# Performance work log

Measured on AMD Instinct MI355X. Metric: run time of the kernel, lower is better.

The kernel has to match this reference:

```python
import jax, jax.numpy as jnp
import numpy as np
from jax import lax

DN = ('NCHW', 'OIHW', 'NCHW')


def conv_s2(x, w, b):
    # Conv2d(kernel=4, stride=2, padding=1): halves H,W
    y = lax.conv_general_dilated(x, w, (2, 2), ((1, 1), (1, 1)), dimension_numbers=DN)
    return y + b[None, :, None, None]


def conv_1x1(x, w, b):
    y = lax.conv_general_dilated(x, w, (1, 1), ((0, 0), (0, 0)), dimension_numbers=DN)
    return y + b[None, :, None, None]


def convT_s2(x, w, b):
    # torch ConvTranspose2d(kernel=4, stride=2, padding=1); torch weight layout [I,O,kh,kw]
    wt = jnp.flip(w, (2, 3)).transpose(1, 0, 2, 3)  # -> [O,I,kh,kw], spatially flipped
    y = lax.conv_general_dilated(x, wt, (1, 1), ((2, 2), (2, 2)),
                                 lhs_dilation=(2, 2), dimension_numbers=DN)
    return y + b[None, :, None, None]


def setup_inputs() -> dict:
    key = jax.random.key(0)
    ks = jax.random.split(key, 20)
    f32 = jnp.float32
    s = 0.05  # small init scale to keep activations sane
    inp = {
        'x': jax.random.uniform(ks[0], (32, 3, 256, 256), dtype=f32),
        # encoder
        'ew1': jax.random.normal(ks[1], (128, 3, 4, 4), f32) * s,
        'eb1': jnp.zeros((128,), f32),
        'ew2': jax.random.normal(ks[2], (256, 128, 4, 4), f32) * s,
        'eb2': jnp.zeros((256,), f32),
        'ew3': jax.random.normal(ks[3], (512, 256, 4, 4), f32) * s,
        'eb3': jnp.zeros((512,), f32),
        # pre-VQ 1x1 conv
        'pw': jax.random.normal(ks[4], (64, 512, 1, 1), f32) * s,
        'pb': jnp.zeros((64,), f32),
        # codebook (torch.randn in module)
        'emb': jax.random.normal(ks[5], (512, 64), f32),
        # decoder (ConvTranspose2d weights: [in, out, kh, kw])
        'dw1': jax.random.normal(ks[6], (64, 256, 4, 4), f32) * s,
        'db1': jnp.zeros((256,), f32),
        'dw2': jax.random.normal(ks[7], (256, 128, 4, 4), f32) * s,
        'db2': jnp.zeros((128,), f32),
        'dw3': jax.random.normal(ks[8], (128, 3, 4, 4), f32) * s,
        'db3': jnp.zeros((3,), f32),
    }
    return inp


def reference(x, ew1, eb1, ew2, eb2, ew3, eb3, pw, pb, emb,
              dw1, db1, dw2, db2, dw3, db3):
    # encoder
    h = jax.nn.relu(conv_s2(x, ew1, eb1))
    h = jax.nn.relu(conv_s2(h, ew2, eb2))
    h = jax.nn.relu(conv_s2(h, ew3, eb3))
    z_e = conv_1x1(h, pw, pb)  # [B, D, H, W]

    b, d, hh, ww = z_e.shape
    x_flat = z_e.reshape(b, d, hh * ww).transpose(0, 2, 1)  # [B, HW, D]
    # squared distances via expansion (same math, no [B,HW,K,D] blowup)
    x2 = jnp.sum(x_flat ** 2, axis=-1, keepdims=True)        # [B, HW, 1]
    e2 = jnp.sum(emb ** 2, axis=-1)                          # [K]
    dist = x2 - 2.0 * jnp.einsum('bnd,kd->bnk', x_flat, emb) + e2[None, None, :]
    indices = jnp.argmin(dist, axis=2)                       # [B, HW]
    zq_flat = emb[indices]                                   # [B, HW, D]
    z_q = zq_flat.transpose(0, 2, 1).reshape(b, d, hh, ww)

    quant_loss = (jnp.mean((zq_flat - x_flat) ** 2) * 2.0)   # matches detach-symmetric mse in fwd value

    # decoder
    y = jax.nn.relu(convT_s2(z_q, dw1, db1))
    y = jax.nn.relu(convT_s2(y, dw2, db2))
    y = jax.nn.sigmoid(convT_s2(y, dw3, db3))
    return (y, quant_loss)
```

## Files before the change

### kernel.cpp

```cpp
#include <hip/hip_runtime.h>
#include <cstddef>

typedef __attribute__((ext_vector_type(8))) _Float16 half8;
typedef __attribute__((ext_vector_type(4))) float f32x4;

static __device__ __forceinline__ unsigned packhl(float v) {
  _Float16 h = (_Float16)v;
  _Float16 l = (_Float16)((v - (float)h) * 2048.0f);
  return (unsigned)__builtin_bit_cast(unsigned short, h) |
         ((unsigned)__builtin_bit_cast(unsigned short, l) << 16);
}


template<int CIN>
__global__ __launch_bounds__(256) void wsplit_k(
    const float* __restrict__ W, _Float16* __restrict__ Wh,
    _Float16* __restrict__ Wl, int Cout) {
  constexpr int NCB = CIN / 32;
  int idx = blockIdx.x * 256 + threadIdx.x;
  if (idx >= Cout * CIN) return;
  int ci = idx % CIN, co = idx / CIN;
  int cb = ci >> 5, k8 = (ci >> 3) & 3, j = ci & 7;
  const float* wp = W + (size_t)idx * 16;
#pragma unroll
  for (int tap = 0; tap < 16; ++tap) {
    float w = wp[tap];
    _Float16 wh = (_Float16)w;
    _Float16 wl = (_Float16)((w - (float)wh) * 2048.0f);
    size_t o = (((size_t)(tap * NCB + cb) * 4 + k8) * Cout + co) * 8 + j;
    Wh[o] = wh; Wl[o] = wl;
  }
}

template<int CIN>
__global__ __launch_bounds__(256) void wsplitT_k(
    const float* __restrict__ W, _Float16* __restrict__ Wh,
    _Float16* __restrict__ Wl, int Cout) {
  constexpr int NCB = CIN / 32;
  int idx = blockIdx.x * 256 + threadIdx.x;
  if (idx >= CIN * Cout) return;
  int co = idx % Cout, ci = idx / Cout;
  int cb = ci >> 5, k8 = (ci >> 3) & 3, j = ci & 7;
  const float* wp = W + (size_t)idx * 16;
#pragma unroll
  for (int t = 0; t < 16; ++t) {
    int py = (t >> 3) & 1, px = (t >> 2) & 1, i0 = (t >> 1) & 1, i1 = t & 1;
    int kh = py ? (i0 ? 2 : 0) : (i0 ? 3 : 1);
    int kw = px ? (i1 ? 2 : 0) : (i1 ? 3 : 1);
    float w = wp[kh * 4 + kw];
    _Float16 wh = (_Float16)w;
    _Float16 wl = (_Float16)((w - (float)wh) * 2048.0f);
    size_t o = (((size_t)(t * NCB + cb) * 4 + k8) * Cout + co) * 8 + j;
    Wh[o] = wh; Wl[o] = wl;
  }
}

template<int CIN, int COUT, int CGRP, int NF, int RELU, int PACKOUT>
__global__ __launch_bounds__(256) void conv_mfma2(
    const unsigned* __restrict__ inU, const _Float16* __restrict__ Whg,
    const _Float16* __restrict__ Wlg, const float* __restrict__ bias,
    float* __restrict__ out, int Hin, int Win) {
  constexpr int NCB  = CIN / 32;
  constexpr int MT   = COUT / CGRP;
  constexpr int MF   = MT / 64;
  constexpr int ROWS = 2 * NF + 2;
  constexpr int NPOS = ROWS * 34;
  constexpr int K8S  = NPOS + 6;
  const int Hout = Hin >> 1, Wout = Win >> 1;
  const int TW = Wout >> 4;
  __shared__ half8 Bh[4 * K8S], Bl[4 * K8S];
  const int tid = threadIdx.x;
  const int lane = tid & 63, w = tid >> 6;
  const int l15 = lane & 15, k8 = lane >> 4;
  const int tx = blockIdx.x % TW, ty = blockIdx.x / TW;
  const int cg = blockIdx.y % CGRP;
  const int b  = blockIdx.y / CGRP;
  const int oy0 = ty * NF, ox0 = tx << 4;
  const int iy_org = 2 * oy0 - 1, ix_org = 2 * ox0 - 1;
  const int cbase = cg * MT + w * (MT / 4);
  const size_t HW = (size_t)Hin * Win;
  const size_t tapStride = (size_t)NCB * 4 * COUT * 8;

  f32x4 accM[MF][NF], accX[MF][NF];
#pragma unroll
  for (int m = 0; m < MF; ++m)
#pragma unroll
    for (int nf = 0; nf < NF; ++nf) {
      accM[m][nf] = f32x4{0,0,0,0};
      accX[m][nf] = f32x4{0,0,0,0};
    }

  for (int cb = 0; cb < NCB; ++cb) {
    __syncthreads();
    for (int u = tid; u < NPOS * 4; u += 256) {
      int kk = u / NPOS, pos = u - kk * NPOS;
      int hy = pos / 34, hx = pos - hy * 34;
      int iy = iy_org + hy, ix = ix_org + hx;
      bool ok = (unsigned)iy < (unsigned)Hin && (unsigned)ix < (unsigned)Win;
      uint4 qa = {0,0,0,0}, qb = {0,0,0,0};
      if (ok) {
        const uint4* gp = (const uint4*)(inU +
            (((size_t)b * (CIN / 8) + cb * 4 + kk) * HW + (size_t)iy * Win + ix) * 8);
        qa = gp[0]; qb = gp[1];
      }
      unsigned av[8] = {qa.x, qa.y, qa.z, qa.w, qb.x, qb.y, qb.z, qb.w};
      half8 vh, vl;
#pragma unroll
      for (int j = 0; j < 8; ++j) {
        vh[j] = __builtin_bit_cast(_Float16, (unsigned short)(av[j] & 0xffffu));
        vl[j] = __builtin_bit_cast(_Float16, (unsigned short)(av[j] >> 16));
      }
      int slotBase = (hy * 2 + (hx & 1)) * 17 + (hx >> 1);
      Bh[kk * K8S + slotBase] = vh;
      Bl[kk * K8S + slotBase] = vl;
    }
    __syncthreads();
    const _Float16* aph = Whg + (((size_t)cb * 4 + k8) * COUT + cbase + l15) * 8;
    const _Float16* apl = Wlg + (((size_t)cb * 4 + k8) * COUT + cbase + l15) * 8;
    half8 ah[2][MF], al[2][MF];
#pragma unroll
    for (int m = 0; m < MF; ++m) {
      ah[0][m] = *(const half8*)(aph + m * 128);
      al[0][m] = *(const half8*)(apl + m * 128);
    }
#pragma unroll
    for (int tp = 0; tp < 16; ++tp) {
      const int cur = tp & 1, nxt = cur ^ 1;
      if (tp < 15) {
#pragma unroll
        for (int m = 0; m < MF; ++m) {
          ah[nxt][m] = *(const half8*)(aph + (size_t)(tp + 1) * tapStride + m * 128);
          al[nxt][m] = *(const half8*)(apl + (size_t)(tp + 1) * tapStride + m * 128);
        }
      }
      const int kh = tp >> 2, kw = tp & 3;
      const int p = kw & 1, cidx = kw >> 1;
#pragma unroll
      for (int nf = 0; nf < NF; ++nf) {
        const int slot = k8 * K8S + ((2 * nf + kh) * 2 + p) * 17 + l15 + cidx;
        const half8 bh = Bh[slot], bl = Bl[slot];
#pragma unroll
        for (int m = 0; m < MF; ++m) {
          accM[m][nf] = __builtin_amdgcn_mfma_f32_16x16x32_f16(ah[cur][m], bh, accM[m][nf], 0, 0, 0);
          accX[m][nf] = __builtin_amdgcn_mfma_f32_16x16x32_f16(ah[cur][m], bl, accX[m][nf], 0, 0, 0);
          accX[m][nf] = __builtin_amdgcn_mfma_f32_16x16x32_f16(al[cur][m], bh, accX[m][nf], 0, 0, 0);
        }
      }
    }
  }
#pragma unroll
  for (int m = 0; m < MF; ++m)
#pragma unroll
    for (int nf = 0; nf < NF; ++nf) {
      int oy = oy0 + nf, ox = ox0 + l15;
      if (PACKOUT) {
        unsigned pk[4];
#pragma unroll
        for (int i = 0; i < 4; ++i) {
          int co = cbase + m * 16 + k8 * 4 + i;
          float v = accM[m][nf][i] + accX[m][nf][i] * (1.0f / 2048.0f) + bias[co];
          if (RELU) v = fmaxf(v, 0.0f);
          pk[i] = packhl(v);
        }
        int co8 = (cbase + m * 16 + k8 * 4) >> 3;
        int j0 = (k8 & 1) * 4;
        unsigned* outU = (unsigned*)out;
        *(uint4*)(outU + (((size_t)b * (COUT / 8) + co8) * ((size_t)Hout * Wout)
                          + (size_t)oy * Wout + ox) * 8 + j0) =
            make_uint4(pk[0], pk[1], pk[2], pk[3]);
      } else {
#pragma unroll
        for (int i = 0; i < 4; ++i) {
          int co = cbase + m * 16 + k8 * 4 + i;
          float v = accM[m][nf][i] + accX[m][nf][i] * (1.0f / 2048.0f) + bias[co];
          if (RELU) v = fmaxf(v, 0.0f);
          out[(((size_t)b * COUT + co) * Hout + oy) * Wout + ox] = v;
        }
      }
    }
}

template<int CIN, int RELU, int PACKIN, int PACKOUT>
__global__ __launch_bounds__(256) void convT_mfma(
    const float* __restrict__ in, const _Float16* __restrict__ Whg,
    const _Float16* __restrict__ Wlg, const float* __restrict__ bias,
    float* __restrict__ out, int Cout, int Hin, int Win) {
  constexpr int NCB = CIN / 32;
  const int Hout = Hin * 2, Wout = Win * 2;
  const int TW = Win >> 4;
  __shared__ half8 Bh[4 * 72], Bl[4 * 72];
  const int tid = threadIdx.x;
  const int lane = tid & 63, w = tid >> 6;
  const int l15 = lane & 15, k8 = lane >> 4;
  const int tx = blockIdx.x % TW, ty = blockIdx.x / TW;
  const int cbo = blockIdx.y % (Cout >> 6);
  const int b   = blockIdx.y / (Cout >> 6);
  const int ty0 = ty << 1, tx0 = tx << 4;
  const int co0 = (cbo << 6) + (w << 4);
  const size_t HW = (size_t)Hin * Win;
  const size_t tapStride = (size_t)NCB * 4 * Cout * 8;

  f32x4 accM[4][2], accX[4][2];
#pragma unroll
  for (int p = 0; p < 4; ++p)
#pragma unroll
    for (int nf = 0; nf < 2; ++nf) {
      accM[p][nf] = f32x4{0,0,0,0};
      accX[p][nf] = f32x4{0,0,0,0};
    }

  for (int cb = 0; cb < NCB; ++cb) {
    __syncthreads();
    for (int u = tid; u < 288; u += 256) {
      int pos = u % 72, kk = u / 72;
      int r = pos / 18, c = pos - r * 18;
      int iy = ty0 - 1 + r, ix = tx0 - 1 + c;
      bool ok = (unsigned)iy < (unsigned)Hin && (unsigned)ix < (unsigned)Win;
      half8 vh, vl;
      if (PACKIN) {
        uint4 qa = {0,0,0,0}, qb = {0,0,0,0};
        if (ok) {
          const uint4* gp = (const uint4*)((const unsigned*)in +
              (((size_t)b * (CIN / 8) + cb * 4 + kk) * HW + (size_t)iy * Win + ix) * 8);
          qa = gp[0]; qb = gp[1];
        }
        unsigned av[8] = {qa.x, qa.y, qa.z, qa.w, qb.x, qb.y, qb.z, qb.w};
#pragma unroll
        for (int j = 0; j < 8; ++j) {
          vh[j] = __builtin_bit_cast(_Float16, (unsigned short)(av[j] & 0xffffu));
          vl[j] = __builtin_bit_cast(_Float16, (unsigned short)(av[j] >> 16));
        }
      } else {
        const float* gp = in + ((size_t)b * CIN + cb * 32 + kk * 8) * HW
                          + (ptrdiff_t)iy * Win + ix;
#pragma unroll
        for (int j = 0; j < 8; ++j) {
          float x = ok ? gp[(size_t)j * HW] : 0.0f;
          _Float16 xh = (_Float16)x;
          vh[j] = xh; vl[j] = (_Float16)((x - (float)xh) * 2048.0f);
        }
      }
      Bh[kk * 72 + pos] = vh;
      Bl[kk * 72 + pos] = vl;
    }
    __syncthreads();
    const _Float16* aph = Whg + (((size_t)cb * 4 + k8) * Cout + co0 + l15) * 8;
    const _Float16* apl = Wlg + (((size_t)cb * 4 + k8) * Cout + co0 + l15) * 8;
    half8 ahA = *(const half8*)(aph);
    half8 alA = *(const half8*)(apl);
#pragma unroll
    for (int t = 0; t < 16; ++t) {
      half8 ahN, alN;
      if (t < 15) {
        ahN = *(const half8*)(aph + (size_t)(t + 1) * tapStride);
        alN = *(const half8*)(apl + (size_t)(t + 1) * tapStride);
      }
      const int py = (t >> 3) & 1, px = (t >> 2) & 1;
      const int i0 = (t >> 1) & 1, i1 = t & 1;
      const int dy = py ? (i0 ? 0 : 1) : (i0 ? -1 : 0);
      const int dx = px ? (i1 ? 0 : 1) : (i1 ? -1 : 0);
      const int p = py * 2 + px;
#pragma unroll
      for (int nf = 0; nf < 2; ++nf) {
        int slot = k8 * 72 + (nf + 1 + dy) * 18 + (l15 + 1 + dx);
        half8 bh = Bh[slot], bl = Bl[slot];
        accM[p][nf] = __builtin_amdgcn_mfma_f32_16x16x32_f16(ahA, bh, accM[p][nf], 0, 0, 0);
        accX[p][nf] = __builtin_amdgcn_mfma_f32_16x16x32_f16(ahA, bl, accX[p][nf], 0, 0, 0);
        accX[p][nf] = __builtin_amdgcn_mfma_f32_16x16x32_f16(alA, bh, accX[p][nf], 0, 0, 0);
      }
      if (t < 15) { ahA = ahN; alA = alN; }
    }
  }
#pragma unroll
  for (int nf = 0; nf < 2; ++nf) {
#pragma unroll
    for (int i = 0; i < 4; ++i) {
      int co = co0 + k8 * 4 + i;
      float bb = bias[co];
#pragma unroll
      for (int py = 0; py < 2; ++py) {
        float v0 = accM[py * 2 + 0][nf][i] + accX[py * 2 + 0][nf][i] * (1.0f / 2048.0f) + bb;
        float v1 = accM[py * 2 + 1][nf][i] + accX[py * 2 + 1][nf][i] * (1.0f / 2048.0f) + bb;
        if (RELU) { v0 = fmaxf(v0, 0.0f); v1 = fmaxf(v1, 0.0f); }
        int oy = 2 * (ty0 + nf) + py, ox = 2 * (tx0 + l15);
        if (PACKOUT) {
          unsigned* outU = (unsigned*)out;
          int co8 = (co0 >> 3) + (k8 >> 1);
          int j = (k8 * 4 + i) & 7;
          size_t base = ((size_t)b * (Cout / 8) + co8) * ((size_t)Hout * Wout);
          outU[(base + (size_t)oy * Wout + ox) * 8 + j]     = packhl(v0);
          outU[(base + (size_t)oy * Wout + ox + 1) * 8 + j] = packhl(v1);
        } else {
          *(float2*)(out + (((size_t)b * Cout + co) * Hout + oy) * Wout + ox) =
              make_float2(v0, v1);
        }
      }
    }
  }
}


template<int CIN, int G, int RELU, int PACKOUT>
__global__ __launch_bounds__(256) void conv_t(
    const float* __restrict__ in, const float* __restrict__ wt,
    const float* __restrict__ bias, float* __restrict__ out,
    int Cout, int Hin, int Win) {
  const int Hout = Hin >> 1, Wout = Win >> 1;
  const int TW = Wout >> 4;
  __shared__ float tile[34 * 35];
  int tid = threadIdx.x;
  int oxl = tid & 15, oyl = tid >> 4;
  int tyt = blockIdx.x / TW, txt = blockIdx.x - tyt * TW;
  int oy0 = tyt << 4, ox0 = txt << 4;
  int cg = blockIdx.y % (Cout / G);
  int b  = blockIdx.y / (Cout / G);
  int co0 = cg * G;
  const int iy_org = 2 * oy0 - 1, ix_org = 2 * ox0 - 1;
  const float* ip = in + (size_t)b * CIN * Hin * Win;
  float acc[G];
#pragma unroll
  for (int j = 0; j < G; ++j) acc[j] = bias[co0 + j];
  const int lbase = (2 * oyl) * 35 + 2 * oxl;
  for (int ci = 0; ci < CIN; ++ci) {
    const float* ic = ip + (size_t)ci * Hin * Win;
    __syncthreads();
#pragma unroll
    for (int k = 0; k < 5; ++k) {
      int idx = tid + k * 256;
      if (idx < 34 * 34) {
        int r = idx / 34, c = idx - r * 34;
        int iy = iy_org + r, ix = ix_org + c;
        float v = ((unsigned)iy < (unsigned)Hin && (unsigned)ix < (unsigned)Win)
                      ? ic[(size_t)iy * Win + ix] : 0.0f;
        tile[r * 35 + c] = v;
      }
    }
    __syncthreads();
    float xv[16];
#pragma unroll
    for (int kh = 0; kh < 4; ++kh)
#pragma unroll
      for (int kw = 0; kw < 4; ++kw)
        xv[kh * 4 + kw] = tile[lbase + kh * 35 + kw];
    const float* wc = wt + ((size_t)co0 * CIN + ci) * 16;
#pragma unroll
    for (int j = 0; j < G; ++j) {
      const float* wj = wc + (size_t)j * CIN * 16;
#pragma unroll
      for (int t2 = 0; t2 < 16; ++t2) acc[j] = fmaf(xv[t2], wj[t2], acc[j]);
    }
  }
  int oy = oy0 + oyl, ox = ox0 + oxl;
  if (RELU) {
#pragma unroll
    for (int j = 0; j < G; ++j) acc[j] = fmaxf(acc[j], 0.0f);
  }
  if (PACKOUT) {
    unsigned* outU = (unsigned*)out;
    size_t cs = (size_t)Hout * Wout;
#pragma unroll
    for (int mb = 0; mb < G / 8; ++mb) {
      unsigned pk[8];
#pragma unroll
      for (int j = 0; j < 8; ++j) pk[j] = packhl(acc[mb * 8 + j]);
      size_t base = (((size_t)b * (Cout / 8) + (co0 >> 3) + mb) * cs
                     + (size_t)oy * Wout + ox) * 8;
      *(uint4*)(outU + base)     = make_uint4(pk[0], pk[1], pk[2], pk[3]);
      *(uint4*)(outU + base + 4) = make_uint4(pk[4], pk[5], pk[6], pk[7]);
    }
  } else {
    size_t cs = (size_t)Hout * Wout;
    float* op = out + ((size_t)(b * Cout + co0) * Hout + oy) * Wout + ox;
#pragma unroll
    for (int j = 0; j < G; ++j) op[(size_t)j * cs] = acc[j];
  }
}

template<int CIN, int G>
__global__ __launch_bounds__(256) void conv1x1_k(
    const float* __restrict__ in, const float* __restrict__ wt,
    const float* __restrict__ bias, float* __restrict__ out,
    int Cout, int HW) {
  int hw = blockIdx.x * 256 + threadIdx.x;
  int cg = blockIdx.y % (Cout / G);
  int b  = blockIdx.y / (Cout / G);
  int co0 = cg * G;
  const float* ip = in + (size_t)b * CIN * HW + hw;
  float acc[G];
#pragma unroll
  for (int j = 0; j < G; ++j) acc[j] = bias[co0 + j];
#pragma unroll 4
  for (int ci = 0; ci < CIN; ++ci) {
    float xv = ip[(size_t)ci * HW];
#pragma unroll
    for (int j = 0; j < G; ++j)
      acc[j] = fmaf(xv, wt[(size_t)(co0 + j) * CIN + ci], acc[j]);
  }
  float* op = out + ((size_t)(b * Cout + co0)) * HW + hw;
#pragma unroll
  for (int j = 0; j < G; ++j) op[(size_t)j * HW] = acc[j];
}

__global__ __launch_bounds__(128) void vq_k(
    const float* __restrict__ ze, const float* __restrict__ emb,
    float* __restrict__ zq, float* __restrict__ partial) {
  __shared__ float4 se4[128 * 16];
  __shared__ float red[128];
  int tid = threadIdx.x;
  int gid = blockIdx.x * 128 + tid;
  int b = gid >> 10, n = gid & 1023;
  const float* zp = ze + ((size_t)b << 16) + n;
  float4 v4[16];
#pragma unroll
  for (int d = 0; d < 16; ++d) {
    v4[d].x = zp[(size_t)(4 * d + 0) << 10];
    v4[d].y = zp[(size_t)(4 * d + 1) << 10];
    v4[d].z = zp[(size_t)(4 * d + 2) << 10];
    v4[d].w = zp[(size_t)(4 * d + 3) << 10];
  }
  float best = 1e30f; int bi = 0;
  for (int c = 0; c < 4; ++c) {
    __syncthreads();
    for (int i = tid; i < 2048; i += 128)
      se4[i] = ((const float4*)emb)[(c << 11) + i];
    __syncthreads();
    for (int k = 0; k < 128; ++k) {
      const float4* e = se4 + (k << 4);
      float s = 0.0f;
#pragma unroll
      for (int d = 0; d < 16; ++d) {
        float4 ev = e[d];
        float t0 = v4[d].x - ev.x; s = fmaf(t0, t0, s);
        float t1 = v4[d].y - ev.y; s = fmaf(t1, t1, s);
        float t2 = v4[d].z - ev.z; s = fmaf(t2, t2, s);
        float t3 = v4[d].w - ev.w; s = fmaf(t3, t3, s);
      }
      if (s < best) { best = s; bi = (c << 7) + k; }
    }
  }
  const float4* eb4 = (const float4*)emb + ((size_t)bi << 4);
  float* qp = zq + ((size_t)b << 16) + n;
  float ls = 0.0f;
#pragma unroll
  for (int d = 0; d < 16; ++d) {
    float4 q = eb4[d];
    qp[(size_t)(4 * d + 0) << 10] = q.x;
    qp[(size_t)(4 * d + 1) << 10] = q.y;
    qp[(size_t)(4 * d + 2) << 10] = q.z;
    qp[(size_t)(4 * d + 3) << 10] = q.w;
    float t0 = q.x - v4[d].x; ls = fmaf(t0, t0, ls);
    float t1 = q.y - v4[d].y; ls = fmaf(t1, t1, ls);
    float t2 = q.z - v4[d].z; ls = fmaf(t2, t2, ls);
    float t3 = q.w - v4[d].w; ls = fmaf(t3, t3, ls);
  }
  red[tid] = ls;
  __syncthreads();
  for (int s = 64; s > 0; s >>= 1) {
    if (tid < s) red[tid] += red[tid + s];
    __syncthreads();
  }
  if (tid == 0) partial[blockIdx.x] = red[0];
}

__global__ __launch_bounds__(256) void loss_fin(
    const float* __restrict__ partial, float* __restrict__ out) {
  __shared__ float red[256];
  int t = threadIdx.x;
  red[t] = partial[t];
  __syncthreads();
  for (int s = 128; s > 0; s >>= 1) {
    if (t < s) red[t] += red[t + s];
    __syncthreads();
  }
  if (t == 0) out[0] = red[0] * (2.0f / 2097152.0f);
}

template<int CIN, int G, int ACT>
__global__ __launch_bounds__(256) void convT_t(
    const float* __restrict__ in, const float* __restrict__ wt,
    const float* __restrict__ bias, float* __restrict__ out,
    int Cout, int Hin, int Win) {
  const int Hout = Hin * 2, Wout = Win * 2;
  const int TW = Win >> 4;
  __shared__ float tile[18 * 19];
  int tid = threadIdx.x;
  int txl = tid & 15, tyl = tid >> 4;
  int tyt = blockIdx.x / TW, txt = blockIdx.x - tyt * TW;
  int ty0 = tyt << 4, tx0 = txt << 4;
  int og = blockIdx.y % (Cout / G);
  int b  = blockIdx.y / (Cout / G);
  int o0 = og * G;
  const int iy_org = ty0 - 1, ix_org = tx0 - 1;
  const float* ip = in + (size_t)b * CIN * Hin * Win;
  float a00[G], a01[G], a10[G], a11[G];
#pragma unroll
  for (int j = 0; j < G; ++j) {
    float bb = bias[o0 + j];
    a00[j] = bb; a01[j] = bb; a10[j] = bb; a11[j] = bb;
  }
  const int lb = tyl * 19 + txl;
  for (int i = 0; i < CIN; ++i) {
    const float* ic = ip + (size_t)i * Hin * Win;
    __syncthreads();
#pragma unroll
    for (int k = 0; k < 2; ++k) {
      int idx = tid + k * 256;
      if (idx < 18 * 18) {
        int r = idx / 18, c = idx - r * 18;
        int iy = iy_org + r, ix = ix_org + c;
        float v = ((unsigned)iy < (unsigned)Hin && (unsigned)ix < (unsigned)Win)
                      ? ic[(size_t)iy * Win + ix] : 0.0f;
        tile[r * 19 + c] = v;
      }
    }
    __syncthreads();
    float x00 = tile[lb],          x01 = tile[lb + 1],      x02 = tile[lb + 2];
    float x10 = tile[lb + 19],     x11 = tile[lb + 20],     x12 = tile[lb + 21];
    float x20 = tile[lb + 38],     x21 = tile[lb + 39],     x22 = tile[lb + 40];
    const float* wv = wt + ((size_t)i * Cout + o0) * 16;
#pragma unroll
    for (int j = 0; j < G; ++j) {
      const float* w4 = wv + j * 16;
      a00[j] = fmaf(x11, w4[5],  fmaf(x10, w4[7],  fmaf(x01, w4[13], fmaf(x00, w4[15], a00[j]))));
      a01[j] = fmaf(x12, w4[4],  fmaf(x11, w4[6],  fmaf(x02, w4[12], fmaf(x01, w4[14], a01[j]))));
      a10[j] = fmaf(x21, w4[1],  fmaf(x20, w4[3],  fmaf(x11, w4[9],  fmaf(x10, w4[11], a10[j]))));
      a11[j] = fmaf(x22, w4[0],  fmaf(x21, w4[2],  fmaf(x12, w4[8],  fmaf(x11, w4[10], a11[j]))));
    }
  }
  size_t cs = (size_t)Hout * Wout;
  int ty = ty0 + tyl, tx = tx0 + txl;
  size_t base = ((size_t)(b * Cout + o0) * Hout + 2 * (size_t)ty) * Wout + 2 * tx;
#pragma unroll
  for (int j = 0; j < G; ++j) {
    float v00 = a00[j], v01 = a01[j], v10 = a10[j], v11 = a11[j];
    if (ACT == 1) {
      v00 = fmaxf(v00, 0.0f); v01 = fmaxf(v01, 0.0f);
      v10 = fmaxf(v10, 0.0f); v11 = fmaxf(v11, 0.0f);
    } else if (ACT == 2) {
      v00 = 1.0f / (1.0f + expf(-v00)); v01 = 1.0f / (1.0f + expf(-v01));
      v10 = 1.0f / (1.0f + expf(-v10)); v11 = 1.0f / (1.0f + expf(-v11));
    }
    *(float2*)(out + base + (size_t)j * cs)        = make_float2(v00, v01);
    *(float2*)(out + base + (size_t)j * cs + Wout) = make_float2(v10, v11);
  }
}

extern "C" void kernel_launch(void* const* d_in, const int* in_sizes, int n_in,
                              void* d_out, int out_size, void* d_ws, size_t ws_size,
                              hipStream_t stream) {
  const float* x   = (const float*)d_in[0];
  const float* ew1 = (const float*)d_in[1];
  const float* eb1 = (const float*)d_in[2];
  const float* ew2 = (const float*)d_in[3];
  const float* eb2 = (const float*)d_in[4];
  const float* ew3 = (const float*)d_in[5];
  const float* eb3 = (const float*)d_in[6];
  const float* pw  = (const float*)d_in[7];
  const float* pb  = (const float*)d_in[8];
  const float* emb = (const float*)d_in[9];
  const float* dw1 = (const float*)d_in[10];
  const float* db1 = (const float*)d_in[11];
  const float* dw2 = (const float*)d_in[12];
  const float* db2 = (const float*)d_in[13];
  const float* dw3 = (const float*)d_in[14];
  const float* db3 = (const float*)d_in[15];
  float* out = (float*)d_out;
  char* ws = (char*)d_ws;

  const size_t PER  = 13107200ull;
  const size_t WEXT = 4096ull + 13631488ull;
  int CB = 32;
  while (CB > 1 && (size_t)CB * PER + WEXT > ws_size) CB >>= 1;
  const size_t SA = (size_t)CB * 8388608ull;
  const size_t SB = (size_t)CB * 4194304ull;
  const size_t SC = (size_t)CB * 262144ull;
  float* A    = (float*)(ws);
  float* Bp   = (float*)(ws + SA);
  float* ze   = (float*)(ws + SA + SB);
  float* zq   = (float*)(ws + SA + SB + SC);
  float* part = (float*)(ws + SA + SB + 2 * SC);
  _Float16* wh2  = (_Float16*)(ws + SA + SB + 2 * SC + 4096);
  _Float16* wl2  = wh2 + 524288;
  _Float16* wh3  = wl2 + 524288;
  _Float16* wl3  = wh3 + 2097152;
  _Float16* whT1 = wl3 + 2097152;
  _Float16* wlT1 = whT1 + 262144;
  _Float16* whT2 = wlT1 + 262144;
  _Float16* wlT2 = whT2 + 524288;

  wsplit_k<128><<<128, 256, 0, stream>>>(ew2, wh2, wl2, 256);
  wsplit_k<256><<<512, 256, 0, stream>>>(ew3, wh3, wl3, 512);
  wsplitT_k<64><<<64,  256, 0, stream>>>(dw1, whT1, wlT1, 256);
  wsplitT_k<256><<<128, 256, 0, stream>>>(dw2, whT2, wlT2, 128);

  for (int c0 = 0; c0 < 32; c0 += CB) {
    const float* xc = x + (size_t)c0 * 3 * 65536;
    float* outc = out + (size_t)c0 * 3 * 65536;
    conv_t<3, 16, 1, 1><<<dim3(64, CB * 8), 256, 0, stream>>>(xc, ew1, eb1, A, 128, 256, 256);
    conv_mfma2<128, 256, 1, 2, 1, 1><<<dim3(128, CB),    256, 0, stream>>>(
        (const unsigned*)A,  wh2, wl2, eb2, Bp, 128, 128);
    conv_mfma2<256, 512, 2, 2, 1, 0><<<dim3(32, CB * 2), 256, 0, stream>>>(
        (const unsigned*)Bp, wh3, wl3, eb3, A, 64, 64);
    conv1x1_k<512, 4><<<dim3(4, CB * 16), 256, 0, stream>>>(A, pw, pb, ze, 64, 1024);
    vq_k<<<CB * 8, 128, 0, stream>>>(ze, emb, zq, part + (size_t)c0 * 8);
    convT_mfma<64,  1, 0, 1><<<dim3(32,  CB * 4), 256, 0, stream>>>(zq, whT1, wlT1, db1, Bp, 256, 32, 32);
    convT_mfma<256, 1, 1, 0><<<dim3(128, CB * 2), 256, 0, stream>>>(Bp, whT2, wlT2, db2, A, 128, 64, 64);
    convT_t<128, 3, 2><<<dim3(64, CB * 1), 256, 0, stream>>>(A, dw3, db3, outc, 3, 128, 128);
  }
  loss_fin<<<1, 256, 0, stream>>>(part, out + (size_t)(out_size - 1));
}
```

Before: 2.341 ms.

## Store layer-1 activations as padded hi/lo fp16 planes and load via global_load_lds

The first encoder conv now writes its output as separate padded high and low fp16 planes, with a one-pixel zero border filled by a new border kernel. The second encoder conv then stages its input tiles straight from global memory into LDS with global_load_lds, dropping the per-element bounds checks, unpacking and register round trip. Workgroup IDs are also swizzled across the grid to change scheduling locality. In exchange the workspace layout grows, an extra small kernel launch is added, and the chunk size CB may shrink if the workspace is tight.

```diff
diff --git a/kernel.cpp b/kernel.cpp
--- a/kernel.cpp
+++ b/kernel.cpp
@@ -1,5 +1,6 @@
 #include <hip/hip_runtime.h>
 #include <cstddef>
+#include <cstdint>
 
 typedef __attribute__((ext_vector_type(8))) _Float16 half8;
 typedef __attribute__((ext_vector_type(4))) float f32x4;
@@ -55,11 +56,30 @@
   }
 }
 
-template<int CIN, int COUT, int CGRP, int NF, int RELU, int PACKOUT>
+__global__ __launch_bounds__(256) void border_k(
+    char* base, int c8n, int H2, int W2, size_t SAI, size_t LOFF, int nimg) {
+  int nb = 2 * W2 + 2 * (H2 - 2);
+  int tot = nimg * c8n * 2 * nb;
+  int idx = blockIdx.x * 256 + threadIdx.x;
+  if (idx >= tot) return;
+  int s = idx % nb; int r = idx / nb;
+  int pl = r & 1; r >>= 1;
+  int c8 = r % c8n; int b = r / c8n;
+  int y, x;
+  if (s < W2)            { y = 0;       x = s; }
+  else if (s < 2 * W2)   { y = H2 - 1;  x = s - W2; }
+  else { int t = s - 2 * W2; y = 1 + (t >> 1); x = (t & 1) ? W2 - 1 : 0; }
+  size_t PLANE = (size_t)H2 * W2 * 16;
+  char* p = base + (size_t)b * SAI + (size_t)pl * LOFF + (size_t)c8 * PLANE
+            + ((size_t)y * W2 + x) * 16;
+  *(uint4*)p = make_uint4(0, 0, 0, 0);
+}
+
+template<int CIN, int COUT, int CGRP, int NF, int RELU, int PACKOUT, int SPLITIN>
 __global__ __launch_bounds__(256) void conv_mfma2(
-    const unsigned* __restrict__ inU, const _Float16* __restrict__ Whg,
+    const void* __restrict__ inP, const _Float16* __restrict__ Whg,
     const _Float16* __restrict__ Wlg, const float* __restrict__ bias,
-    float* __restrict__ out, int Hin, int Win) {
+    float* __restrict__ out, int Hin, int Win, size_t inSAI, size_t inLOFF) {
   constexpr int NCB  = CIN / 32;
   constexpr int MT   = COUT / CGRP;
   constexpr int MF   = MT / 64;
@@ -72,15 +92,38 @@
   const int tid = threadIdx.x;
   const int lane = tid & 63, w = tid >> 6;
   const int l15 = lane & 15, k8 = lane >> 4;
-  const int tx = blockIdx.x % TW, ty = blockIdx.x / TW;
-  const int cg = blockIdx.y % CGRP;
-  const int b  = blockIdx.y / CGRP;
+  unsigned nwg = gridDim.x * gridDim.y;
+  unsigned id  = blockIdx.y * gridDim.x + blockIdx.x;
+  unsigned sw  = (id & 7) * (nwg >> 3) + (id >> 3);
+  const int bx = sw % gridDim.x, by = sw / gridDim.x;
+  const int tx = bx % TW, ty = bx / TW;
+  const int cg = by % CGRP;
+  const int b  = by / CGRP;
   const int oy0 = ty * NF, ox0 = tx << 4;
   const int iy_org = 2 * oy0 - 1, ix_org = 2 * ox0 - 1;
   const int cbase = cg * MT + w * (MT / 4);
   const size_t HW = (size_t)Hin * Win;
   const size_t tapStride = (size_t)NCB * 4 * COUT * 8;
 
+  unsigned goff[4];
+  const char* baseh = nullptr;
+  size_t PLANE = 0;
+  if (SPLITIN) {
+    const int W2 = Win + 2;
+    PLANE = (size_t)(Hin + 2) * W2 * 16;
+    constexpr int S0[4] = {0, 64, 128, NPOS - 64};
+#pragma unroll
+    for (int t = 0; t < 4; ++t) {
+      int s = S0[t] + lane;
+      int r = s / 17, c = s - r * 17;
+      int hy = r >> 1, p = r & 1;
+      int hx = (c << 1) | p;
+      int iy = iy_org + hy + 1, ix = ix_org + hx + 1;
+      goff[t] = (unsigned)(((size_t)iy * W2 + ix) * 16);
+    }
+    baseh = (const char*)inP + ((size_t)b * inSAI) + (size_t)w * PLANE;
+  }
+
   f32x4 accM[MF][NF], accX[MF][NF];
 #pragma unroll
   for (int m = 0; m < MF; ++m)
@@ -92,27 +135,44 @@
 
   for (int cb = 0; cb < NCB; ++cb) {
     __syncthreads();
-    for (int u = tid; u < NPOS * 4; u += 256) {
-      int kk = u / NPOS, pos = u - kk * NPOS;
-      int hy = pos / 34, hx = pos - hy * 34;
-      int iy = iy_org + hy, ix = ix_org + hx;
-      bool ok = (unsigned)iy < (unsigned)Hin && (unsigned)ix < (unsigned)Win;
-      uint4 qa = {0,0,0,0}, qb = {0,0,0,0};
-      if (ok) {
-        const uint4* gp = (const uint4*)(inU +
-            (((size_t)b * (CIN / 8) + cb * 4 + kk) * HW + (size_t)iy * Win + ix) * 8);
-        qa = gp[0]; qb = gp[1];
-      }
-      unsigned av[8] = {qa.x, qa.y, qa.z, qa.w, qb.x, qb.y, qb.z, qb.w};
-      half8 vh, vl;
-#pragma unroll
-      for (int j = 0; j < 8; ++j) {
-        vh[j] = __builtin_bit_cast(_Float16, (unsigned short)(av[j] & 0xffffu));
-        vl[j] = __builtin_bit_cast(_Float16, (unsigned short)(av[j] >> 16));
-      }
-      int slotBase = (hy * 2 + (hx & 1)) * 17 + (hx >> 1);
-      Bh[kk * K8S + slotBase] = vh;
-      Bl[kk * K8S + slotBase] = vl;
+    if (SPLITIN) {
+      const char* pc = baseh + (size_t)cb * 4 * PLANE;
+      char* lh = (char*)&Bh[w * K8S];
+      char* ll = (char*)&Bl[w * K8S];
+      constexpr int S0[4] = {0, 64, 128, NPOS - 64};
+#pragma unroll
+      for (int t = 0; t < 4; ++t) {
+        __builtin_amdgcn_global_load_lds(
+            (const __attribute__((address_space(1))) void*)(pc + goff[t]),
+            (__attribute__((address_space(3))) void*)(lh + S0[t] * 16), 16, 0, 0);
+        __builtin_amdgcn_global_load_lds(
+            (const __attribute__((address_space(1))) void*)(pc + inLOFF + goff[t]),
+            (__attribute__((address_space(3))) void*)(ll + S0[t] * 16), 16, 0, 0);
+      }
+    } else {
+      const unsigned* inU = (const unsigned*)inP;
+      for (int u = tid; u < NPOS * 4; u += 256) {
+        int kk = u / NPOS, pos = u - kk * NPOS;
+        int hy = pos / 34, hx = pos - hy * 34;
+        int iy = iy_org + hy, ix = ix_org + hx;
+        bool ok = (unsigned)iy < (unsigned)Hin && (unsigned)ix < (unsigned)Win;
+        uint4 qa = {0,0,0,0}, qb = {0,0,0,0};
+        if (ok) {
+          const uint4* gp = (const uint4*)(inU +
+              (((size_t)b * (CIN / 8) + cb * 4 + kk) * HW + (size_t)iy * Win + ix) * 8);
+          qa = gp[0]; qb = gp[1];
+        }
+        unsigned av[8] = {qa.x, qa.y, qa.z, qa.w, qb.x, qb.y, qb.z, qb.w};
+        half8 vh, vl;
+#pragma unroll
+        for (int j = 0; j < 8; ++j) {
+          vh[j] = __builtin_bit_cast(_Float16, (unsigned short)(av[j] & 0xffffu));
+          vl[j] = __builtin_bit_cast(_Float16, (unsigned short)(av[j] >> 16));
+        }
+        int slotBase = (hy * 2 + (hx & 1)) * 17 + (hx >> 1);
+        Bh[kk * K8S + slotBase] = vh;
+        Bl[kk * K8S + slotBase] = vl;
+      }
     }
     __syncthreads();
     const _Float16* aph = Whg + (((size_t)cb * 4 + k8) * COUT + cbase + l15) * 8;
@@ -304,7 +364,7 @@
 __global__ __launch_bounds__(256) void conv_t(
     const float* __restrict__ in, const float* __restrict__ wt,
     const float* __restrict__ bias, float* __restrict__ out,
-    int Cout, int Hin, int Win) {
+    int Cout, int Hin, int Win, size_t oSAI, size_t oLOFF) {
   const int Hout = Hin >> 1, Wout = Win >> 1;
   const int TW = Wout >> 4;
   __shared__ float tile[34 * 35];
@@ -355,18 +415,23 @@
 #pragma unroll
     for (int j = 0; j < G; ++j) acc[j] = fmaxf(acc[j], 0.0f);
   }
-  if (PACKOUT) {
-    unsigned* outU = (unsigned*)out;
-    size_t cs = (size_t)Hout * Wout;
+  if (PACKOUT == 2) {
+    const int W2 = Wout + 2;
+    const size_t PLANE = (size_t)(Hout + 2) * W2 * 16;
+    char* ob0 = (char*)out + (size_t)b * oSAI
+                + ((size_t)(oy + 1) * W2 + ox + 1) * 16;
 #pragma unroll
     for (int mb = 0; mb < G / 8; ++mb) {
-      unsigned pk[8];
-#pragma unroll
-      for (int j = 0; j < 8; ++j) pk[j] = packhl(acc[mb * 8 + j]);
-      size_t base = (((size_t)b * (Cout / 8) + (co0 >> 3) + mb) * cs
-                     + (size_t)oy * Wout + ox) * 8;
-      *(uint4*)(outU + base)     = make_uint4(pk[0], pk[1], pk[2], pk[3]);
-      *(uint4*)(outU + base + 4) = make_uint4(pk[4], pk[5], pk[6], pk[7]);
+      half8 hv, lv;
+#pragma unroll
+      for (int j = 0; j < 8; ++j) {
+        float v = acc[mb * 8 + j];
+        _Float16 h = (_Float16)v;
+        hv[j] = h; lv[j] = (_Float16)((v - (float)h) * 2048.0f);
+      }
+      char* ob = ob0 + (size_t)((co0 >> 3) + mb) * PLANE;
+      *(half8*)ob = hv;
+      *(half8*)(ob + oLOFF) = lv;
     }
   } else {
     size_t cs = (size_t)Hout * Wout;
@@ -567,11 +632,14 @@
   float* out = (float*)d_out;
   char* ws = (char*)d_ws;
 
-  const size_t PER  = 13107200ull;
+  const size_t H1PLANE = 130ull * 130ull * 16ull;
+  const size_t H1LOFF  = 16ull * H1PLANE;
+  const size_t SAI     = 2ull * H1LOFF;
+  const size_t PER  = SAI + 4194304ull + 2ull * 262144ull;
   const size_t WEXT = 4096ull + 13631488ull;
   int CB = 32;
   while (CB > 1 && (size_t)CB * PER + WEXT > ws_size) CB >>= 1;
-  const size_t SA = (size_t)CB * 8388608ull;
+  const size_t SA = (size_t)CB * SAI;
   const size_t SB = (size_t)CB * 4194304ull;
   const size_t SC = (size_t)CB * 262144ull;
   float* A    = (float*)(ws);
@@ -596,11 +664,18 @@
   for (int c0 = 0; c0 < 32; c0 += CB) {
     const float* xc = x + (size_t)c0 * 3 * 65536;
     float* outc = out + (size_t)c0 * 3 * 65536;
-    conv_t<3, 16, 1, 1><<<dim3(64, CB * 8), 256, 0, stream>>>(xc, ew1, eb1, A, 128, 256, 256);
-    conv_mfma2<128, 256, 1, 2, 1, 1><<<dim3(128, CB),    256, 0, stream>>>(
-        (const unsigned*)A,  wh2, wl2, eb2, Bp, 128, 128);
-    conv_mfma2<256, 512, 2, 2, 1, 0><<<dim3(32, CB * 2), 256, 0, stream>>>(
-        (const unsigned*)Bp, wh3, wl3, eb3, A, 64, 64);
+    {
+      int nb = 2 * 130 + 2 * 128;
+      int tot = CB * 16 * 2 * nb;
+      border_k<<<(tot + 255) / 256, 256, 0, stream>>>(
+          (char*)A, 16, 130, 130, SAI, H1LOFF, CB);
+    }
+    conv_t<3, 16, 1, 2><<<dim3(64, CB * 8), 256, 0, stream>>>(
+        xc, ew1, eb1, A, 128, 256, 256, SAI, H1LOFF);
+    conv_mfma2<128, 256, 1, 2, 1, 1, 1><<<dim3(128, CB), 256, 0, stream>>>(
+        (const void*)A, wh2, wl2, eb2, Bp, 128, 128, SAI, H1LOFF);
+    conv_mfma2<256, 512, 2, 2, 1, 0, 0><<<dim3(32, CB * 2), 256, 0, stream>>>(
+        (const void*)Bp, wh3, wl3, eb3, A, 64, 64, 0, 0);
     conv1x1_k<512, 4><<<dim3(4, CB * 16), 256, 0, stream>>>(A, pw, pb, ze, 64, 1024);
     vq_k<<<CB * 8, 128, 0, stream>>>(ze, emb, zq, part + (size_t)c0 * 8);
     convT_mfma<64,  1, 0, 1><<<dim3(32,  CB * 4), 256, 0, stream>>>(zq, whT1, wlT1, db1, Bp, 256, 32, 32);
```

Measured after the change: 2.352 ms. No clear change (+0.5%).
